# Kernel tuning notes

Hardware: AMD Instinct MI355X
Metric: run time of the kernel (lower is better)

Reference implementation:

```python
import jax, jax.numpy as jnp
import numpy as np

H = 4        # num_heads
HD = 64      # head_dim
BD = 40      # bias_dim
QDIM = 256
KDIM = 256
VDIM = 256
NQ = 1024
NK = 1024
NEG = -9e15


def mish(x):
    return x * jnp.tanh(jax.nn.softplus(x))


def layer_norm(x, g, b, eps=1e-5):
    m = jnp.mean(x, axis=-1, keepdims=True)
    v = jnp.var(x, axis=-1, keepdims=True)
    return (x - m) / jnp.sqrt(v + eps) * g + b


def _xavier(key, fi, fo):
    lim = np.sqrt(6.0 / (fi + fo)).astype(np.float32)
    return jax.random.uniform(key, (fi, fo), minval=-lim, maxval=lim, dtype=jnp.float32)


def setup_inputs() -> dict:
    key = jax.random.key(0)
    ks = jax.random.split(key, 12)
    D = H * HD
    inp = {
        'q': jax.random.normal(ks[0], (NQ, QDIM), jnp.float32),
        'k': jax.random.normal(ks[1], (NK, KDIM), jnp.float32),
        'v': jax.random.normal(ks[2], (NK, VDIM), jnp.float32),
        'bias': jax.random.normal(ks[3], (NQ, NK, BD), jnp.float32),
        'mask': jax.random.randint(ks[4], (NQ, NK), 0, 2, jnp.int32),
        # projections (weights stored [in, out]; biases zero-init as in torch code)
        'Wq': _xavier(ks[5], QDIM, D), 'bq': jnp.zeros((D,), jnp.float32),
        'Wk': _xavier(ks[6], KDIM, D), 'bk': jnp.zeros((D,), jnp.float32),
        'Wbias': _xavier(ks[7], BD, H * BD), 'bbias': jnp.zeros((H * BD,), jnp.float32),
        'Wqo': _xavier(ks[8], D, QDIM), 'bqo': jnp.zeros((QDIM,), jnp.float32),
        'Wko': _xavier(ks[9], D, KDIM), 'bko': jnp.zeros((KDIM,), jnp.float32),
        'g_q': jnp.ones((QDIM,), jnp.float32), 'be_q': jnp.zeros((QDIM,), jnp.float32),
        'g_k': jnp.ones((KDIM,), jnp.float32), 'be_k': jnp.zeros((KDIM,), jnp.float32),
        'Wbo': _xavier(ks[10], BD * H, BD), 'bbo': jnp.zeros((BD,), jnp.float32),
    }
    return inp


def reference(q, k, v, bias, mask, Wq, bq, Wk, bk, Wbias, bbias, Wqo, bqo,
              Wko, bko, g_q, be_q, g_k, be_k, Wbo, bbo):
    nq, nk = q.shape[0], k.shape[0]
    # per-head projections: [H, N, HD]
    proj_q = (q @ Wq + bq).reshape(nq, H, HD).transpose(1, 0, 2)
    proj_k = (k @ Wk + bk).reshape(nk, H, HD).transpose(1, 0, 2)
    # values are raw v broadcast over heads (v_proj is unused in original forward)
    proj_v = jnp.broadcast_to(v[None], (H, nk, v.shape[-1]))

    # distance-bias: project then per-head L2 norm -> [H, Nq, Nk]
    biasp = bias @ Wbias + bbias                          # [Nq, Nk, H*BD]
    diffs = jnp.linalg.norm(biasp.reshape(nq, nk, H, BD), axis=-1).transpose(2, 0, 1)

    logits = jnp.einsum('hqd,hkd->hqk', proj_q, proj_k) / np.float32(np.sqrt(HD))
    logits = logits + diffs
    logits = jnp.where(mask[None] == 0, jnp.float32(NEG), logits)
    attn = jax.nn.softmax(logits, axis=-1)
    values = jnp.einsum('hqk,hkv->hqv', attn, proj_v)      # [H, Nq, VDIM]
    values = values.transpose(1, 0, 2).reshape(nq, H * v.shape[-1])

    # note the (N, HD, H) flatten order, matching torch permute(1,2,0).reshape
    pq = proj_q.transpose(1, 2, 0).reshape(nq, HD * H)
    pk = proj_k.transpose(1, 2, 0).reshape(nk, HD * H)
    q_out = layer_norm(q + mish(pq @ Wqo + bqo), g_q, be_q)
    k_out = layer_norm(k + mish(pk @ Wko + bko), g_k, be_k)

    vals_mean = jnp.mean(values, axis=-1, keepdims=True)   # [Nq, 1]
    bias_out = mish(biasp @ Wbo + bbo)                     # [Nq, Nk, BD]
    return (q_out, k_out, vals_mean, bias_out)
```

## Files before the change

kernel.cpp:

```cpp
#include <hip/hip_runtime.h>
#include <hip/hip_bf16.h>
#include <math.h>

#define NEGV -9e15f

typedef short bf16x8 __attribute__((ext_vector_type(8)));
typedef float f32x4 __attribute__((ext_vector_type(4)));

__device__ __forceinline__ unsigned short f2bf(float x) {
  unsigned u = __float_as_uint(x);
  u += 0x7fffu + ((u >> 16) & 1u);
  return (unsigned short)(u >> 16);
}

__device__ __forceinline__ unsigned pk2(float a, float b) {
  __hip_bfloat162 h = __float22bfloat162_rn(make_float2(a, b));
  unsigned u;
  __builtin_memcpy(&u, &h, 4);
  return u;
}

__device__ __forceinline__ float mishf(float x) {
  float u = __expf(fminf(x, 30.0f));
  float n = u * (u + 2.0f);
  return x * __fdividef(n, n + 2.0f);
}

#define KEEP4(v) asm volatile("" : "+v"((v).x), "+v"((v).y), "+v"((v).z), "+v"((v).w))

__global__ void prep_kernel(const float* __restrict__ v, float* __restrict__ s,
                            const float* __restrict__ Wb, const float* __restrict__ bb,
                            const float* __restrict__ Wo, float* __restrict__ M) {
  int bid = blockIdx.x;
  int lane = threadIdx.x;
  if (bid < 1024) {
    float4 a = *reinterpret_cast<const float4*>(v + (size_t)bid * 256 + lane * 4);
    float x = a.x + a.y + a.z + a.w;
    for (int off = 32; off; off >>= 1) x += __shfl_down(x, off);
    if (lane == 0) s[bid] = x;
  } else {
    int i = bid - 1024;
    if (lane >= 40) return;
    float acc = 0.0f;
    for (int k = 0; k < 160; ++k) {
      float w = (i < 40) ? Wb[i * 160 + k] : bb[k];
      acc = fmaf(w, Wo[k * 40 + lane], acc);
    }
    M[i * 40 + lane] = acc;
  }
}

__global__ __launch_bounds__(256, 2) void gemm_mfma_pair(
    const float* __restrict__ A0, const float* __restrict__ W0,
    const float* __restrict__ bv0, float* __restrict__ C0,
    const float* __restrict__ A1, const float* __restrict__ W1,
    const float* __restrict__ bv1, float* __restrict__ C1, int perm) {
  const float* A = blockIdx.z ? A1 : A0;
  const float* W = blockIdx.z ? W1 : W0;
  const float* bvec = blockIdx.z ? bv1 : bv0;
  float* C = blockIdx.z ? C1 : C0;
  __shared__ unsigned short wT[4 * 8 * 64 * 8];
  int tid = threadIdx.x;
  int wv = tid >> 6, lane = tid & 63;
  int r = lane & 15, g = lane >> 4;
  int c0 = blockIdx.x * 64, r0 = blockIdx.y * 64;

  for (int idx = tid; idx < 4 * 8 * 64; idx += 256) {
    int grp = idx >> 6, lid = idx & 63;
    int n = grp >> 3, ks = grp & 7;
    int cc = c0 + n * 16 + (lid & 15);
    int kbase = ks * 32 + (lid >> 4) * 8;
    unsigned short tmp[8];
#pragma unroll
    for (int jj = 0; jj < 8; ++jj) {
      int k = kbase + jj;
      int row = perm ? ((k & 63) * 4 + (k >> 6)) : k;
      tmp[jj] = f2bf(W[row * 256 + cc]);
    }
    *reinterpret_cast<uint4*>(&wT[idx * 8]) = *reinterpret_cast<const uint4*>(tmp);
  }
  const float* xr = A + (size_t)(r0 + wv * 16 + r) * 256 + g * 8;
  float4 xa[8], xb[8];
#pragma unroll
  for (int ks = 0; ks < 8; ++ks) {
    xa[ks] = *reinterpret_cast<const float4*>(xr + ks * 32);
    xb[ks] = *reinterpret_cast<const float4*>(xr + ks * 32 + 4);
  }
  f32x4 acc[4];
#pragma unroll
  for (int n = 0; n < 4; ++n) {
    float4 b4 = *reinterpret_cast<const float4*>(bvec + c0 + n * 16 + 4 * g);
    acc[n][0] = b4.x; acc[n][1] = b4.y; acc[n][2] = b4.z; acc[n][3] = b4.w;
  }
  __syncthreads();
#pragma unroll
  for (int ks = 0; ks < 8; ++ks) {
    bf16x8 xf;
    uint4 t = {pk2(xa[ks].x, xa[ks].y), pk2(xa[ks].z, xa[ks].w),
               pk2(xb[ks].x, xb[ks].y), pk2(xb[ks].z, xb[ks].w)};
    __builtin_memcpy(&xf, &t, 16);
#pragma unroll
    for (int n = 0; n < 4; ++n) {
      bf16x8 wf = *reinterpret_cast<const bf16x8*>(&wT[((n * 8 + ks) * 64 + lane) * 8]);
      acc[n] = __builtin_amdgcn_mfma_f32_16x16x32_bf16(wf, xf, acc[n], 0, 0, 0);
    }
  }
  float* cp = C + (size_t)(r0 + wv * 16 + r) * 256 + c0;
#pragma unroll
  for (int n = 0; n < 4; ++n) {
    float4 o = {acc[n][0], acc[n][1], acc[n][2], acc[n][3]};
    *reinterpret_cast<float4*>(cp + n * 16 + 4 * g) = o;
  }
}

__global__ __launch_bounds__(256) void ln_pair(
    const float* __restrict__ x0q, const float* __restrict__ yq,
    const float* __restrict__ gq, const float* __restrict__ beq,
    float* __restrict__ outq,
    const float* __restrict__ x0k, const float* __restrict__ yk,
    const float* __restrict__ gk, const float* __restrict__ bek,
    float* __restrict__ outk) {
  const float* x0 = blockIdx.y ? x0k : x0q;
  const float* y  = blockIdx.y ? yk  : yq;
  const float* g  = blockIdx.y ? gk  : gq;
  const float* be = blockIdx.y ? bek : beq;
  float* out      = blockIdx.y ? outk : outq;
  __shared__ float r1[5], r2[5];
  int r = blockIdx.x, t = threadIdx.x;
  int wid = t >> 6, lane = t & 63;
  float x = x0[(size_t)r * 256 + t] + mishf(y[(size_t)r * 256 + t]);
  float a = x, b = x * x;
  for (int off = 32; off; off >>= 1) {
    a += __shfl_down(a, off);
    b += __shfl_down(b, off);
  }
  if (lane == 0) { r1[wid] = a; r2[wid] = b; }
  __syncthreads();
  if (t == 0) {
    r1[4] = r1[0] + r1[1] + r1[2] + r1[3];
    r2[4] = r2[0] + r2[1] + r2[2] + r2[3];
  }
  __syncthreads();
  float m = r1[4] * (1.0f / 256.0f);
  float var = r2[4] * (1.0f / 256.0f) - m * m;
  out[(size_t)r * 256 + t] = (x - m) * rsqrtf(var + 1e-5f) * g[t] + be[t];
}

__global__ __launch_bounds__(256, 4) void bias_mfma(
    const float* __restrict__ bias, const float* __restrict__ Wb,
    const float* __restrict__ bb, const float* __restrict__ Mmat,
    const float* __restrict__ bo, float* __restrict__ diffs,
    float* __restrict__ bout) {
  __shared__ unsigned short wfL[20 * 64 * 8];
  __shared__ unsigned short mfL[6 * 64 * 8];
  int tid = threadIdx.x;
  int wv = tid >> 6, lane = tid & 63;
  int r = lane & 15, g = lane >> 4;

  for (int idx = tid; idx < 20 * 64; idx += 256) {
    int grp = idx >> 6, lid = idx & 63;
    int n0 = grp >> 1, ks = grp & 1;
    int rr = lid & 15, gg = lid >> 4;
    int c = n0 * 16 + rr;
    unsigned short tmp[8];
#pragma unroll
    for (int jj = 0; jj < 8; ++jj) {
      int k = ks * 32 + gg * 8 + jj;
      float w = (k < 40) ? Wb[k * 160 + c] : ((k == 40) ? bb[c] : 0.0f);
      tmp[jj] = f2bf(w);
    }
    *reinterpret_cast<uint4*>(&wfL[idx * 8]) = *reinterpret_cast<const uint4*>(tmp);
  }
  for (int idx = tid; idx < 6 * 64; idx += 256) {
    int grp = idx >> 6, lid = idx & 63;
    int n = grp >> 1, ks = grp & 1;
    int rr = lid & 15, gg = lid >> 4;
    int c = n * 16 + rr;
    unsigned short tmp[8];
#pragma unroll
    for (int jj = 0; jj < 8; ++jj) {
      int k = ks * 32 + gg * 8 + jj;
      float w = (k <= 40 && c < 40) ? Mmat[k * 40 + c] : 0.0f;
      tmp[jj] = f2bf(w);
    }
    *reinterpret_cast<uint4*>(&mfL[idx * 8]) = *reinterpret_cast<const uint4*>(tmp);
  }
  f32x4 bo40, bo41, bo42;
  {
    float4 t0 = *reinterpret_cast<const float4*>(bo + 4 * g);
    float4 t1 = *reinterpret_cast<const float4*>(bo + 16 + 4 * g);
    bo40[0] = t0.x; bo40[1] = t0.y; bo40[2] = t0.z; bo40[3] = t0.w;
    bo41[0] = t1.x; bo41[1] = t1.y; bo41[2] = t1.z; bo41[3] = t1.w;
    if (g < 2) {
      float4 t2 = *reinterpret_cast<const float4*>(bo + 32 + 4 * g);
      bo42[0] = t2.x; bo42[1] = t2.y; bo42[2] = t2.z; bo42[3] = t2.w;
    } else {
      bo42[0] = 0.0f; bo42[1] = 0.0f; bo42[2] = 0.0f; bo42[3] = 0.0f;
    }
  }
  __syncthreads();

  size_t row0 = ((size_t)blockIdx.x * 4 + wv) * 256;

  const float* xr = bias + (row0 + r) * 40;
  float4 xA = *reinterpret_cast<const float4*>(xr + g * 8);
  float4 xB = *reinterpret_cast<const float4*>(xr + g * 8 + 4);
  float4 xC = *reinterpret_cast<const float4*>(xr + 32);
  float4 xD = *reinterpret_cast<const float4*>(xr + 36);
  KEEP4(xA); KEEP4(xB); KEEP4(xC); KEEP4(xD);

#pragma unroll 1
  for (int t = 0; t < 16; ++t) {
    const size_t p0 = row0 + (size_t)t * 16;
    bf16x8 xf0, xf1;
    {
      uint4 t0 = {pk2(xA.x, xA.y), pk2(xA.z, xA.w), pk2(xB.x, xB.y), pk2(xB.z, xB.w)};
      unsigned d0 = (g == 1) ? 0x00003f80u : pk2(xC.x, xC.y);
      uint4 t1 = {d0, pk2(xC.z, xC.w), pk2(xD.x, xD.y), pk2(xD.z, xD.w)};
      __builtin_memcpy(&xf0, &t0, 16);
      __builtin_memcpy(&xf1, &t1, 16);
    }
    if (t < 15) {
      const float* xr2 = bias + (p0 + 16 + r) * 40;
      xA = *reinterpret_cast<const float4*>(xr2 + g * 8);
      xB = *reinterpret_cast<const float4*>(xr2 + g * 8 + 4);
      xC = *reinterpret_cast<const float4*>(xr2 + 32);
      xD = *reinterpret_cast<const float4*>(xr2 + 36);
      KEEP4(xA); KEEP4(xB); KEEP4(xC); KEEP4(xD);
    }
    float cs[10];
#pragma unroll
    for (int n0 = 0; n0 < 10; ++n0) {
      bf16x8 wa = *reinterpret_cast<const bf16x8*>(&wfL[((n0 * 2 + 0) * 64 + lane) * 8]);
      bf16x8 wb2 = *reinterpret_cast<const bf16x8*>(&wfL[((n0 * 2 + 1) * 64 + lane) * 8]);
      f32x4 q = {0.0f, 0.0f, 0.0f, 0.0f};
      q = __builtin_amdgcn_mfma_f32_16x16x32_bf16(wa, xf0, q, 0, 0, 0);
      q = __builtin_amdgcn_mfma_f32_16x16x32_bf16(wb2, xf1, q, 0, 0, 0);
      cs[n0] = q[0] * q[0] + q[1] * q[1] + q[2] * q[2] + q[3] * q[3];
    }
    float hv0 = cs[0] + cs[1] + ((g < 2) ? cs[2] : 0.0f);
    float hv1 = ((g < 2) ? 0.0f : cs[2]) + cs[3] + cs[4];
    float hv2 = cs[5] + cs[6] + ((g < 2) ? cs[7] : 0.0f);
    float hv3 = ((g < 2) ? 0.0f : cs[7]) + cs[8] + cs[9];
    hv0 += __shfl_xor(hv0, 16); hv0 += __shfl_xor(hv0, 32);
    hv1 += __shfl_xor(hv1, 16); hv1 += __shfl_xor(hv1, 32);
    hv2 += __shfl_xor(hv2, 16); hv2 += __shfl_xor(hv2, 32);
    hv3 += __shfl_xor(hv3, 16); hv3 += __shfl_xor(hv3, 32);
    float ss = (g == 0) ? hv0 : (g == 1) ? hv1 : (g == 2) ? hv2 : hv3;
    diffs[(size_t)g * (1024 * 1024) + p0 + r] = sqrtf(ss);
    f32x4 o0 = bo40, o1 = bo41, o2 = bo42;
    {
      bf16x8 m00 = *reinterpret_cast<const bf16x8*>(&mfL[((0 * 2 + 0) * 64 + lane) * 8]);
      bf16x8 m01 = *reinterpret_cast<const bf16x8*>(&mfL[((0 * 2 + 1) * 64 + lane) * 8]);
      bf16x8 m10 = *reinterpret_cast<const bf16x8*>(&mfL[((1 * 2 + 0) * 64 + lane) * 8]);
      bf16x8 m11 = *reinterpret_cast<const bf16x8*>(&mfL[((1 * 2 + 1) * 64 + lane) * 8]);
      bf16x8 m20 = *reinterpret_cast<const bf16x8*>(&mfL[((2 * 2 + 0) * 64 + lane) * 8]);
      bf16x8 m21 = *reinterpret_cast<const bf16x8*>(&mfL[((2 * 2 + 1) * 64 + lane) * 8]);
      o0 = __builtin_amdgcn_mfma_f32_16x16x32_bf16(m00, xf0, o0, 0, 0, 0);
      o1 = __builtin_amdgcn_mfma_f32_16x16x32_bf16(m10, xf0, o1, 0, 0, 0);
      o2 = __builtin_amdgcn_mfma_f32_16x16x32_bf16(m20, xf0, o2, 0, 0, 0);
      o0 = __builtin_amdgcn_mfma_f32_16x16x32_bf16(m01, xf1, o0, 0, 0, 0);
      o1 = __builtin_amdgcn_mfma_f32_16x16x32_bf16(m11, xf1, o1, 0, 0, 0);
      o2 = __builtin_amdgcn_mfma_f32_16x16x32_bf16(m21, xf1, o2, 0, 0, 0);
    }
    float* bp = bout + (size_t)(p0 + r) * 40;
    float4 st;
    st.x = mishf(o0[0]); st.y = mishf(o0[1]);
    st.z = mishf(o0[2]); st.w = mishf(o0[3]);
    *reinterpret_cast<float4*>(bp + 4 * g) = st;
    st.x = mishf(o1[0]); st.y = mishf(o1[1]);
    st.z = mishf(o1[2]); st.w = mishf(o1[3]);
    *reinterpret_cast<float4*>(bp + 16 + 4 * g) = st;
    if (g < 2) {
      st.x = mishf(o2[0]); st.y = mishf(o2[1]);
      st.z = mishf(o2[2]); st.w = mishf(o2[3]);
      *reinterpret_cast<float4*>(bp + 32 + 4 * g) = st;
    }
  }
}

__global__ __launch_bounds__(256) void qk_softmax(
    const float* __restrict__ pq, const float* __restrict__ pk,
    const int* __restrict__ mask, const float* __restrict__ diffs,
    const float* __restrict__ sv, float* __restrict__ mpart,
    float* __restrict__ spart, float* __restrict__ dpart) {
  __shared__ float sQT[64][68];
  __shared__ float sKT[64][68];
  int tid = threadIdx.x;
  int k0 = blockIdx.x * 64, q0 = blockIdx.y * 64, h = blockIdx.z;
  for (int i = tid; i < 1024; i += 256) {
    int r = i >> 4, dq = i & 15;
    float4 a = *reinterpret_cast<const float4*>(pq + (size_t)(q0 + r) * 256 + h * 64 + dq * 4);
    sQT[dq * 4 + 0][r] = a.x;
    sQT[dq * 4 + 1][r] = a.y;
    sQT[dq * 4 + 2][r] = a.z;
    sQT[dq * 4 + 3][r] = a.w;
    float4 b = *reinterpret_cast<const float4*>(pk + (size_t)(k0 + r) * 256 + h * 64 + dq * 4);
    sKT[dq * 4 + 0][r] = b.x;
    sKT[dq * 4 + 1][r] = b.y;
    sKT[dq * 4 + 2][r] = b.z;
    sKT[dq * 4 + 3][r] = b.w;
  }
  __syncthreads();
  int ty = tid >> 4, tx = tid & 15;
  float acc[4][4] = {};
#pragma unroll 4
  for (int d = 0; d < 64; ++d) {
    float4 av = *reinterpret_cast<const float4*>(&sQT[d][ty * 4]);
    float4 bv = *reinterpret_cast<const float4*>(&sKT[d][tx * 4]);
    float a[4] = {av.x, av.y, av.z, av.w};
    float b[4] = {bv.x, bv.y, bv.z, bv.w};
#pragma unroll
    for (int i = 0; i < 4; ++i)
#pragma unroll
      for (int j = 0; j < 4; ++j) acc[i][j] = fmaf(a[i], b[j], acc[i][j]);
  }
  float4 s4 = *reinterpret_cast<const float4*>(sv + k0 + tx * 4);
#pragma unroll
  for (int i = 0; i < 4; ++i) {
    int qq = q0 + ty * 4 + i;
    size_t base = (size_t)h * 1048576 + (size_t)qq * 1024 + k0 + tx * 4;
    float4 dv = *reinterpret_cast<const float4*>(diffs + base);
    int4 mv = *reinterpret_cast<const int4*>(mask + (size_t)qq * 1024 + k0 + tx * 4);
    float l0 = mv.x ? fmaf(acc[i][0], 0.125f, dv.x) : NEGV;
    float l1 = mv.y ? fmaf(acc[i][1], 0.125f, dv.y) : NEGV;
    float l2 = mv.z ? fmaf(acc[i][2], 0.125f, dv.z) : NEGV;
    float l3 = mv.w ? fmaf(acc[i][3], 0.125f, dv.w) : NEGV;
    float tm = fmaxf(fmaxf(l0, l1), fmaxf(l2, l3));
    tm = fmaxf(tm, __shfl_xor(tm, 1));
    tm = fmaxf(tm, __shfl_xor(tm, 2));
    tm = fmaxf(tm, __shfl_xor(tm, 4));
    tm = fmaxf(tm, __shfl_xor(tm, 8));
    float e0 = mv.x ? __expf(l0 - tm) : 0.0f;
    float e1 = mv.y ? __expf(l1 - tm) : 0.0f;
    float e2 = mv.z ? __expf(l2 - tm) : 0.0f;
    float e3 = mv.w ? __expf(l3 - tm) : 0.0f;
    float ps = e0 + e1 + e2 + e3;
    float pd = e0 * s4.x + e1 * s4.y + e2 * s4.z + e3 * s4.w;
    ps += __shfl_xor(ps, 1); pd += __shfl_xor(pd, 1);
    ps += __shfl_xor(ps, 2); pd += __shfl_xor(pd, 2);
    ps += __shfl_xor(ps, 4); pd += __shfl_xor(pd, 4);
    ps += __shfl_xor(ps, 8); pd += __shfl_xor(pd, 8);
    if (tx == 0) {
      int plane = (h * 16 + blockIdx.x) * 1024 + qq;
      mpart[plane] = tm;
      spart[plane] = ps;
      dpart[plane] = pd;
    }
  }
}

__global__ void vm_reduce(const float* __restrict__ mpart,
                          const float* __restrict__ spart,
                          const float* __restrict__ dpart,
                          float* __restrict__ vm) {
  int q = blockIdx.x * 256 + threadIdx.x;
  float accum = 0.0f;
#pragma unroll
  for (int h = 0; h < 4; ++h) {
    float M = -3e38f;
#pragma unroll
    for (int kb = 0; kb < 16; ++kb)
      M = fmaxf(M, mpart[(h * 16 + kb) * 1024 + q]);
    float s = 0.0f, d = 0.0f;
#pragma unroll
    for (int kb = 0; kb < 16; ++kb) {
      int p = (h * 16 + kb) * 1024 + q;
      float sc = __expf(mpart[p] - M);
      s = fmaf(spart[p], sc, s);
      d = fmaf(dpart[p], sc, d);
    }
    accum += d / s;
  }
  vm[q] = accum * (1.0f / 1024.0f);
}

extern "C" void kernel_launch(void* const* d_in, const int* in_sizes, int n_in,
                              void* d_out, int out_size, void* d_ws, size_t ws_size,
                              hipStream_t stream) {
  const float* q     = (const float*)d_in[0];
  const float* k     = (const float*)d_in[1];
  const float* v     = (const float*)d_in[2];
  const float* bias  = (const float*)d_in[3];
  const int*   mask  = (const int*)d_in[4];
  const float* Wq    = (const float*)d_in[5];
  const float* bq    = (const float*)d_in[6];
  const float* Wk    = (const float*)d_in[7];
  const float* bk    = (const float*)d_in[8];
  const float* Wbias = (const float*)d_in[9];
  const float* bbias = (const float*)d_in[10];
  const float* Wqo   = (const float*)d_in[11];
  const float* bqo   = (const float*)d_in[12];
  const float* Wko   = (const float*)d_in[13];
  const float* bko   = (const float*)d_in[14];
  const float* g_q   = (const float*)d_in[15];
  const float* be_q  = (const float*)d_in[16];
  const float* g_k   = (const float*)d_in[17];
  const float* be_k  = (const float*)d_in[18];
  const float* Wbo   = (const float*)d_in[19];
  const float* bbo   = (const float*)d_in[20];

  float* out = (float*)d_out;
  float* ws  = (float*)d_ws;
  float* projq = ws;
  float* projk = ws + 262144;
  float* qo    = ws + 524288;
  float* ko    = ws + 786432;
  float* diffs = ws + 1048576;
  float* svec  = ws + 5242880;
  float* Mmat  = ws + 5243904;
  float* mpart = ws + 5246976;
  float* spart = ws + 5312512;
  float* dpart = ws + 5378048;

  float* q_out    = out;
  float* k_out    = out + 262144;
  float* vmean    = out + 524288;
  float* bias_out = out + 525312;

  prep_kernel<<<1065, 64, 0, stream>>>(v, svec, Wbias, bbias, Wbo, Mmat);
  gemm_mfma_pair<<<dim3(4, 16, 2), 256, 0, stream>>>(q, Wq, bq, projq,
                                                     k, Wk, bk, projk, 0);
  bias_mfma<<<1024, 256, 0, stream>>>(bias, Wbias, bbias, Mmat, bbo, diffs, bias_out);
  gemm_mfma_pair<<<dim3(4, 16, 2), 256, 0, stream>>>(projq, Wqo, bqo, qo,
                                                     projk, Wko, bko, ko, 1);
  ln_pair<<<dim3(1024, 2), 256, 0, stream>>>(q, qo, g_q, be_q, q_out,
                                             k, ko, g_k, be_k, k_out);
  qk_softmax<<<dim3(16, 16, 4), 256, 0, stream>>>(projq, projk, mask, diffs,
                                                  svec, mpart, spart, dpart);
  vm_reduce<<<4, 256, 0, stream>>>(mpart, spart, dpart, vmean);
}
```

Before: 141.0 us.

## Use bf16 MFMA for QK logits and double-buffer bias prefetch

The qk_softmax kernel drops its fp32 shared-memory FMA outer product. K tiles are converted to bf16 in LDS, Q fragments are held in registers, and the logits come from 16x16x32 bf16 MFMA, with the softmax reductions restructured to match the MFMA output layout. The bias_mfma loop is unrolled by two with two register buffers, so each tile's loads are issued two iterations ahead. Both changes aim to cut ALU/LDS time and hide global load latency, at the cost of bf16 precision in the logits and higher register pressure.

New measurement: 143.0 us. No clear change (+1.4%).

```diff
diff --git a/kernel.cpp b/kernel.cpp
--- a/kernel.cpp
+++ b/kernel.cpp
@@ -146,6 +146,75 @@
   out[(size_t)r * 256 + t] = (x - m) * rsqrtf(var + 1e-5f) * g[t] + be[t];
 }
 
+#define TILE5(XA, XB, XC, XD, T) do {                                                  \
+    const size_t p0 = row0 + (size_t)(T) * 16;                                         \
+    bf16x8 xf0, xf1;                                                                   \
+    {                                                                                  \
+      uint4 t0 = {pk2((XA).x, (XA).y), pk2((XA).z, (XA).w),                            \
+                  pk2((XB).x, (XB).y), pk2((XB).z, (XB).w)};                           \
+      unsigned d0 = (g == 1) ? 0x00003f80u : pk2((XC).x, (XC).y);                      \
+      uint4 t1 = {d0, pk2((XC).z, (XC).w), pk2((XD).x, (XD).y), pk2((XD).z, (XD).w)};  \
+      __builtin_memcpy(&xf0, &t0, 16);                                                 \
+      __builtin_memcpy(&xf1, &t1, 16);                                                 \
+    }                                                                                  \
+    if ((T) + 2 < 16) {                                                                \
+      const float* xr2 = bias + (p0 + 32 + r) * 40;                                    \
+      XA = *reinterpret_cast<const float4*>(xr2 + g * 8);                              \
+      XB = *reinterpret_cast<const float4*>(xr2 + g * 8 + 4);                          \
+      XC = *reinterpret_cast<const float4*>(xr2 + 32);                                 \
+      XD = *reinterpret_cast<const float4*>(xr2 + 36);                                 \
+      KEEP4(XA); KEEP4(XB); KEEP4(XC); KEEP4(XD);                                      \
+    }                                                                                  \
+    float cs[10];                                                                      \
+    _Pragma("unroll")                                                                  \
+    for (int n0 = 0; n0 < 10; ++n0) {                                                  \
+      bf16x8 wa = *reinterpret_cast<const bf16x8*>(&wfL[((n0 * 2 + 0) * 64 + lane) * 8]); \
+      bf16x8 wb2 = *reinterpret_cast<const bf16x8*>(&wfL[((n0 * 2 + 1) * 64 + lane) * 8]); \
+      f32x4 q = {0.0f, 0.0f, 0.0f, 0.0f};                                              \
+      q = __builtin_amdgcn_mfma_f32_16x16x32_bf16(wa, xf0, q, 0, 0, 0);                \
+      q = __builtin_amdgcn_mfma_f32_16x16x32_bf16(wb2, xf1, q, 0, 0, 0);               \
+      cs[n0] = q[0] * q[0] + q[1] * q[1] + q[2] * q[2] + q[3] * q[3];                  \
+    }                                                                                  \
+    float hv0 = cs[0] + cs[1] + ((g < 2) ? cs[2] : 0.0f);                              \
+    float hv1 = ((g < 2) ? 0.0f : cs[2]) + cs[3] + cs[4];                              \
+    float hv2 = cs[5] + cs[6] + ((g < 2) ? cs[7] : 0.0f);                              \
+    float hv3 = ((g < 2) ? 0.0f : cs[7]) + cs[8] + cs[9];                              \
+    hv0 += __shfl_xor(hv0, 16); hv0 += __shfl_xor(hv0, 32);                            \
+    hv1 += __shfl_xor(hv1, 16); hv1 += __shfl_xor(hv1, 32);                            \
+    hv2 += __shfl_xor(hv2, 16); hv2 += __shfl_xor(hv2, 32);                            \
+    hv3 += __shfl_xor(hv3, 16); hv3 += __shfl_xor(hv3, 32);                            \
+    float ss = (g == 0) ? hv0 : (g == 1) ? hv1 : (g == 2) ? hv2 : hv3;                 \
+    diffs[(size_t)g * (1024 * 1024) + p0 + r] = sqrtf(ss);                             \
+    f32x4 o0 = bo40, o1 = bo41, o2 = bo42;                                             \
+    {                                                                                  \
+      bf16x8 m00 = *reinterpret_cast<const bf16x8*>(&mfL[((0 * 2 + 0) * 64 + lane) * 8]); \
+      bf16x8 m01 = *reinterpret_cast<const bf16x8*>(&mfL[((0 * 2 + 1) * 64 + lane) * 8]); \
+      bf16x8 m10 = *reinterpret_cast<const bf16x8*>(&mfL[((1 * 2 + 0) * 64 + lane) * 8]); \
+      bf16x8 m11 = *reinterpret_cast<const bf16x8*>(&mfL[((1 * 2 + 1) * 64 + lane) * 8]); \
+      bf16x8 m20 = *reinterpret_cast<const bf16x8*>(&mfL[((2 * 2 + 0) * 64 + lane) * 8]); \
+      bf16x8 m21 = *reinterpret_cast<const bf16x8*>(&mfL[((2 * 2 + 1) * 64 + lane) * 8]); \
+      o0 = __builtin_amdgcn_mfma_f32_16x16x32_bf16(m00, xf0, o0, 0, 0, 0);             \
+      o1 = __builtin_amdgcn_mfma_f32_16x16x32_bf16(m10, xf0, o1, 0, 0, 0);             \
+      o2 = __builtin_amdgcn_mfma_f32_16x16x32_bf16(m20, xf0, o2, 0, 0, 0);             \
+      o0 = __builtin_amdgcn_mfma_f32_16x16x32_bf16(m01, xf1, o0, 0, 0, 0);             \
+      o1 = __builtin_amdgcn_mfma_f32_16x16x32_bf16(m11, xf1, o1, 0, 0, 0);             \
+      o2 = __builtin_amdgcn_mfma_f32_16x16x32_bf16(m21, xf1, o2, 0, 0, 0);             \
+    }                                                                                  \
+    float* bp = bout + (size_t)(p0 + r) * 40;                                          \
+    float4 st;                                                                         \
+    st.x = mishf(o0[0]); st.y = mishf(o0[1]);                                          \
+    st.z = mishf(o0[2]); st.w = mishf(o0[3]);                                          \
+    *reinterpret_cast<float4*>(bp + 4 * g) = st;                                       \
+    st.x = mishf(o1[0]); st.y = mishf(o1[1]);                                          \
+    st.z = mishf(o1[2]); st.w = mishf(o1[3]);                                          \
+    *reinterpret_cast<float4*>(bp + 16 + 4 * g) = st;                                  \
+    if (g < 2) {                                                                       \
+      st.x = mishf(o2[0]); st.y = mishf(o2[1]);                                        \
+      st.z = mishf(o2[2]); st.w = mishf(o2[3]);                                        \
+      *reinterpret_cast<float4*>(bp + 32 + 4 * g) = st;                                \
+    }                                                                                  \
+  } while (0)
+
 __global__ __launch_bounds__(256, 4) void bias_mfma(
     const float* __restrict__ bias, const float* __restrict__ Wb,
     const float* __restrict__ bb, const float* __restrict__ Mmat,
@@ -202,80 +271,23 @@
 
   size_t row0 = ((size_t)blockIdx.x * 4 + wv) * 256;
 
-  const float* xr = bias + (row0 + r) * 40;
-  float4 xA = *reinterpret_cast<const float4*>(xr + g * 8);
-  float4 xB = *reinterpret_cast<const float4*>(xr + g * 8 + 4);
-  float4 xC = *reinterpret_cast<const float4*>(xr + 32);
-  float4 xD = *reinterpret_cast<const float4*>(xr + 36);
-  KEEP4(xA); KEEP4(xB); KEEP4(xC); KEEP4(xD);
+  const float* xr0 = bias + (row0 + r) * 40;
+  const float* xr1 = bias + (row0 + 16 + r) * 40;
+  float4 x0A = *reinterpret_cast<const float4*>(xr0 + g * 8);
+  float4 x0B = *reinterpret_cast<const float4*>(xr0 + g * 8 + 4);
+  float4 x0C = *reinterpret_cast<const float4*>(xr0 + 32);
+  float4 x0D = *reinterpret_cast<const float4*>(xr0 + 36);
+  float4 x1A = *reinterpret_cast<const float4*>(xr1 + g * 8);
+  float4 x1B = *reinterpret_cast<const float4*>(xr1 + g * 8 + 4);
+  float4 x1C = *reinterpret_cast<const float4*>(xr1 + 32);
+  float4 x1D = *reinterpret_cast<const float4*>(xr1 + 36);
+  KEEP4(x0A); KEEP4(x0B); KEEP4(x0C); KEEP4(x0D);
+  KEEP4(x1A); KEEP4(x1B); KEEP4(x1C); KEEP4(x1D);
 
 #pragma unroll 1
-  for (int t = 0; t < 16; ++t) {
-    const size_t p0 = row0 + (size_t)t * 16;
-    bf16x8 xf0, xf1;
-    {
-      uint4 t0 = {pk2(xA.x, xA.y), pk2(xA.z, xA.w), pk2(xB.x, xB.y), pk2(xB.z, xB.w)};
-      unsigned d0 = (g == 1) ? 0x00003f80u : pk2(xC.x, xC.y);
-      uint4 t1 = {d0, pk2(xC.z, xC.w), pk2(xD.x, xD.y), pk2(xD.z, xD.w)};
-      __builtin_memcpy(&xf0, &t0, 16);
-      __builtin_memcpy(&xf1, &t1, 16);
-    }
-    if (t < 15) {
-      const float* xr2 = bias + (p0 + 16 + r) * 40;
-      xA = *reinterpret_cast<const float4*>(xr2 + g * 8);
-      xB = *reinterpret_cast<const float4*>(xr2 + g * 8 + 4);
-      xC = *reinterpret_cast<const float4*>(xr2 + 32);
-      xD = *reinterpret_cast<const float4*>(xr2 + 36);
-      KEEP4(xA); KEEP4(xB); KEEP4(xC); KEEP4(xD);
-    }
-    float cs[10];
-#pragma unroll
-    for (int n0 = 0; n0 < 10; ++n0) {
-      bf16x8 wa = *reinterpret_cast<const bf16x8*>(&wfL[((n0 * 2 + 0) * 64 + lane) * 8]);
-      bf16x8 wb2 = *reinterpret_cast<const bf16x8*>(&wfL[((n0 * 2 + 1) * 64 + lane) * 8]);
-      f32x4 q = {0.0f, 0.0f, 0.0f, 0.0f};
-      q = __builtin_amdgcn_mfma_f32_16x16x32_bf16(wa, xf0, q, 0, 0, 0);
-      q = __builtin_amdgcn_mfma_f32_16x16x32_bf16(wb2, xf1, q, 0, 0, 0);
-      cs[n0] = q[0] * q[0] + q[1] * q[1] + q[2] * q[2] + q[3] * q[3];
-    }
-    float hv0 = cs[0] + cs[1] + ((g < 2) ? cs[2] : 0.0f);
-    float hv1 = ((g < 2) ? 0.0f : cs[2]) + cs[3] + cs[4];
-    float hv2 = cs[5] + cs[6] + ((g < 2) ? cs[7] : 0.0f);
-    float hv3 = ((g < 2) ? 0.0f : cs[7]) + cs[8] + cs[9];
-    hv0 += __shfl_xor(hv0, 16); hv0 += __shfl_xor(hv0, 32);
-    hv1 += __shfl_xor(hv1, 16); hv1 += __shfl_xor(hv1, 32);
-    hv2 += __shfl_xor(hv2, 16); hv2 += __shfl_xor(hv2, 32);
-    hv3 += __shfl_xor(hv3, 16); hv3 += __shfl_xor(hv3, 32);
-    float ss = (g == 0) ? hv0 : (g == 1) ? hv1 : (g == 2) ? hv2 : hv3;
-    diffs[(size_t)g * (1024 * 1024) + p0 + r] = sqrtf(ss);
-    f32x4 o0 = bo40, o1 = bo41, o2 = bo42;
-    {
-      bf16x8 m00 = *reinterpret_cast<const bf16x8*>(&mfL[((0 * 2 + 0) * 64 + lane) * 8]);
-      bf16x8 m01 = *reinterpret_cast<const bf16x8*>(&mfL[((0 * 2 + 1) * 64 + lane) * 8]);
-      bf16x8 m10 = *reinterpret_cast<const bf16x8*>(&mfL[((1 * 2 + 0) * 64 + lane) * 8]);
-      bf16x8 m11 = *reinterpret_cast<const bf16x8*>(&mfL[((1 * 2 + 1) * 64 + lane) * 8]);
-      bf16x8 m20 = *reinterpret_cast<const bf16x8*>(&mfL[((2 * 2 + 0) * 64 + lane) * 8]);
-      bf16x8 m21 = *reinterpret_cast<const bf16x8*>(&mfL[((2 * 2 + 1) * 64 + lane) * 8]);
-      o0 = __builtin_amdgcn_mfma_f32_16x16x32_bf16(m00, xf0, o0, 0, 0, 0);
-      o1 = __builtin_amdgcn_mfma_f32_16x16x32_bf16(m10, xf0, o1, 0, 0, 0);
-      o2 = __builtin_amdgcn_mfma_f32_16x16x32_bf16(m20, xf0, o2, 0, 0, 0);
-      o0 = __builtin_amdgcn_mfma_f32_16x16x32_bf16(m01, xf1, o0, 0, 0, 0);
-      o1 = __builtin_amdgcn_mfma_f32_16x16x32_bf16(m11, xf1, o1, 0, 0, 0);
-      o2 = __builtin_amdgcn_mfma_f32_16x16x32_bf16(m21, xf1, o2, 0, 0, 0);
-    }
-    float* bp = bout + (size_t)(p0 + r) * 40;
-    float4 st;
-    st.x = mishf(o0[0]); st.y = mishf(o0[1]);
-    st.z = mishf(o0[2]); st.w = mishf(o0[3]);
-    *reinterpret_cast<float4*>(bp + 4 * g) = st;
-    st.x = mishf(o1[0]); st.y = mishf(o1[1]);
-    st.z = mishf(o1[2]); st.w = mishf(o1[3]);
-    *reinterpret_cast<float4*>(bp + 16 + 4 * g) = st;
-    if (g < 2) {
-      st.x = mishf(o2[0]); st.y = mishf(o2[1]);
-      st.z = mishf(o2[2]); st.w = mishf(o2[3]);
-      *reinterpret_cast<float4*>(bp + 32 + 4 * g) = st;
-    }
+  for (int t = 0; t < 16; t += 2) {
+    TILE5(x0A, x0B, x0C, x0D, t);
+    TILE5(x1A, x1B, x1C, x1D, t + 1);
   }
 }
 
@@ -284,69 +296,86 @@
     const int* __restrict__ mask, const float* __restrict__ diffs,
     const float* __restrict__ sv, float* __restrict__ mpart,
     float* __restrict__ spart, float* __restrict__ dpart) {
-  __shared__ float sQT[64][68];
-  __shared__ float sKT[64][68];
+  __shared__ unsigned short kT[8 * 64 * 8];
   int tid = threadIdx.x;
+  int wv = tid >> 6, lane = tid & 63;
+  int r = lane & 15, g = lane >> 4;
   int k0 = blockIdx.x * 64, q0 = blockIdx.y * 64, h = blockIdx.z;
-  for (int i = tid; i < 1024; i += 256) {
-    int r = i >> 4, dq = i & 15;
-    float4 a = *reinterpret_cast<const float4*>(pq + (size_t)(q0 + r) * 256 + h * 64 + dq * 4);
-    sQT[dq * 4 + 0][r] = a.x;
-    sQT[dq * 4 + 1][r] = a.y;
-    sQT[dq * 4 + 2][r] = a.z;
-    sQT[dq * 4 + 3][r] = a.w;
-    float4 b = *reinterpret_cast<const float4*>(pk + (size_t)(k0 + r) * 256 + h * 64 + dq * 4);
-    sKT[dq * 4 + 0][r] = b.x;
-    sKT[dq * 4 + 1][r] = b.y;
-    sKT[dq * 4 + 2][r] = b.z;
-    sKT[dq * 4 + 3][r] = b.w;
-  }
+
+  for (int idx = tid; idx < 8 * 64; idx += 256) {
+    int grp = idx >> 6, lid = idx & 63;
+    int n = grp >> 1, ks = grp & 1;
+    int cc = n * 16 + (lid & 15);
+    int dbase = ks * 32 + (lid >> 4) * 8;
+    const float* kp = pk + (size_t)(k0 + cc) * 256 + h * 64 + dbase;
+    unsigned short tmp[8];
+#pragma unroll
+    for (int jj = 0; jj < 8; ++jj) tmp[jj] = f2bf(kp[jj]);
+    *reinterpret_cast<uint4*>(&kT[idx * 8]) = *reinterpret_cast<const uint4*>(tmp);
+  }
+  int qq = q0 + wv * 16 + r;
+  const float* qp = pq + (size_t)qq * 256 + h * 64;
+  float4 qa0 = *reinterpret_cast<const float4*>(qp + g * 8);
+  float4 qb0 = *reinterpret_cast<const float4*>(qp + g * 8 + 4);
+  float4 qa1 = *reinterpret_cast<const float4*>(qp + 32 + g * 8);
+  float4 qb1 = *reinterpret_cast<const float4*>(qp + 32 + g * 8 + 4);
+  float4 s4[4];
+#pragma unroll
+  for (int n = 0; n < 4; ++n)
+    s4[n] = *reinterpret_cast<const float4*>(sv + k0 + n * 16 + 4 * g);
   __syncthreads();
-  int ty = tid >> 4, tx = tid & 15;
-  float acc[4][4] = {};
-#pragma unroll 4
-  for (int d = 0; d < 64; ++d) {
-    float4 av = *reinterpret_cast<const float4*>(&sQT[d][ty * 4]);
-    float4 bv = *reinterpret_cast<const float4*>(&sKT[d][tx * 4]);
-    float a[4] = {av.x, av.y, av.z, av.w};
-    float b[4] = {bv.x, bv.y, bv.z, bv.w};
-#pragma unroll
-    for (int i = 0; i < 4; ++i)
-#pragma unroll
-      for (int j = 0; j < 4; ++j) acc[i][j] = fmaf(a[i], b[j], acc[i][j]);
-  }
-  float4 s4 = *reinterpret_cast<const float4*>(sv + k0 + tx * 4);
-#pragma unroll
-  for (int i = 0; i < 4; ++i) {
-    int qq = q0 + ty * 4 + i;
-    size_t base = (size_t)h * 1048576 + (size_t)qq * 1024 + k0 + tx * 4;
+
+  bf16x8 xf0, xf1;
+  {
+    uint4 t0 = {pk2(qa0.x, qa0.y), pk2(qa0.z, qa0.w), pk2(qb0.x, qb0.y), pk2(qb0.z, qb0.w)};
+    uint4 t1 = {pk2(qa1.x, qa1.y), pk2(qa1.z, qa1.w), pk2(qb1.x, qb1.y), pk2(qb1.z, qb1.w)};
+    __builtin_memcpy(&xf0, &t0, 16);
+    __builtin_memcpy(&xf1, &t1, 16);
+  }
+  f32x4 acc[4];
+#pragma unroll
+  for (int n = 0; n < 4; ++n) {
+    f32x4 z = {0.0f, 0.0f, 0.0f, 0.0f};
+    bf16x8 k0f = *reinterpret_cast<const bf16x8*>(&kT[((n * 2 + 0) * 64 + lane) * 8]);
+    bf16x8 k1f = *reinterpret_cast<const bf16x8*>(&kT[((n * 2 + 1) * 64 + lane) * 8]);
+    z = __builtin_amdgcn_mfma_f32_16x16x32_bf16(k0f, xf0, z, 0, 0, 0);
+    acc[n] = __builtin_amdgcn_mfma_f32_16x16x32_bf16(k1f, xf1, z, 0, 0, 0);
+  }
+  f32x4 l[4];
+  float tm = -3e38f;
+#pragma unroll
+  for (int n = 0; n < 4; ++n) {
+    size_t base = (size_t)h * 1048576 + (size_t)qq * 1024 + k0 + n * 16 + 4 * g;
     float4 dv = *reinterpret_cast<const float4*>(diffs + base);
-    int4 mv = *reinterpret_cast<const int4*>(mask + (size_t)qq * 1024 + k0 + tx * 4);
-    float l0 = mv.x ? fmaf(acc[i][0], 0.125f, dv.x) : NEGV;
-    float l1 = mv.y ? fmaf(acc[i][1], 0.125f, dv.y) : NEGV;
-    float l2 = mv.z ? fmaf(acc[i][2], 0.125f, dv.z) : NEGV;
-    float l3 = mv.w ? fmaf(acc[i][3], 0.125f, dv.w) : NEGV;
-    float tm = fmaxf(fmaxf(l0, l1), fmaxf(l2, l3));
-    tm = fmaxf(tm, __shfl_xor(tm, 1));
-    tm = fmaxf(tm, __shfl_xor(tm, 2));
-    tm = fmaxf(tm, __shfl_xor(tm, 4));
-    tm = fmaxf(tm, __shfl_xor(tm, 8));
-    float e0 = mv.x ? __expf(l0 - tm) : 0.0f;
-    float e1 = mv.y ? __expf(l1 - tm) : 0.0f;
-    float e2 = mv.z ? __expf(l2 - tm) : 0.0f;
-    float e3 = mv.w ? __expf(l3 - tm) : 0.0f;
-    float ps = e0 + e1 + e2 + e3;
-    float pd = e0 * s4.x + e1 * s4.y + e2 * s4.z + e3 * s4.w;
-    ps += __shfl_xor(ps, 1); pd += __shfl_xor(pd, 1);
-    ps += __shfl_xor(ps, 2); pd += __shfl_xor(pd, 2);
-    ps += __shfl_xor(ps, 4); pd += __shfl_xor(pd, 4);
-    ps += __shfl_xor(ps, 8); pd += __shfl_xor(pd, 8);
-    if (tx == 0) {
-      int plane = (h * 16 + blockIdx.x) * 1024 + qq;
-      mpart[plane] = tm;
-      spart[plane] = ps;
-      dpart[plane] = pd;
-    }
+    int4 mv = *reinterpret_cast<const int4*>(mask + (size_t)qq * 1024 + k0 + n * 16 + 4 * g);
+    l[n][0] = mv.x ? fmaf(acc[n][0], 0.125f, dv.x) : NEGV;
+    l[n][1] = mv.y ? fmaf(acc[n][1], 0.125f, dv.y) : NEGV;
+    l[n][2] = mv.z ? fmaf(acc[n][2], 0.125f, dv.z) : NEGV;
+    l[n][3] = mv.w ? fmaf(acc[n][3], 0.125f, dv.w) : NEGV;
+    tm = fmaxf(tm, fmaxf(fmaxf(l[n][0], l[n][1]), fmaxf(l[n][2], l[n][3])));
+  }
+  tm = fmaxf(tm, __shfl_xor(tm, 16));
+  tm = fmaxf(tm, __shfl_xor(tm, 32));
+  float ps = 0.0f, pd = 0.0f;
+#pragma unroll
+  for (int n = 0; n < 4; ++n) {
+    float e0 = (l[n][0] > -1e15f) ? __expf(l[n][0] - tm) : 0.0f;
+    float e1 = (l[n][1] > -1e15f) ? __expf(l[n][1] - tm) : 0.0f;
+    float e2 = (l[n][2] > -1e15f) ? __expf(l[n][2] - tm) : 0.0f;
+    float e3 = (l[n][3] > -1e15f) ? __expf(l[n][3] - tm) : 0.0f;
+    ps += e0 + e1 + e2 + e3;
+    pd = fmaf(e0, s4[n].x, pd);
+    pd = fmaf(e1, s4[n].y, pd);
+    pd = fmaf(e2, s4[n].z, pd);
+    pd = fmaf(e3, s4[n].w, pd);
+  }
+  ps += __shfl_xor(ps, 16); pd += __shfl_xor(pd, 16);
+  ps += __shfl_xor(ps, 32); pd += __shfl_xor(pd, 32);
+  if (g == 0) {
+    int plane = (h * 16 + blockIdx.x) * 1024 + qq;
+    mpart[plane] = tm;
+    spart[plane] = ps;
+    dpart[plane] = pd;
   }
 }
 
```
